# Performance work log

Measured on AMD Instinct MI355X. Metric: run time of the kernel, lower is better.

## Reference

```python
import jax, jax.numpy as jnp
import numpy as np

D_MODEL = 1024
NUM_HEADS = 16
D_K = D_MODEL // NUM_HEADS
LN_EPS = 1e-5
NEG = -1e9


def setup_inputs() -> dict:
    key = jax.random.key(0)
    ks = jax.random.split(key, 12)
    B, S, D = 8, 1024, D_MODEL
    lim = 1.0 / np.sqrt(D)
    def lin(k):
        k1, k2 = jax.random.split(k)
        W = jax.random.uniform(k1, (D, D), jnp.float32, -lim, lim)
        b = jax.random.uniform(k2, (D,), jnp.float32, -lim, lim)
        return W, b
    Wq, bq = lin(ks[0])
    Wk, bk = lin(ks[1])
    Wv, bv = lin(ks[2])
    Wo, bo = lin(ks[3])
    return {
        "history_items": jax.random.normal(ks[4], (B, S, D), jnp.float32),
        "sequence_mask": jax.random.randint(ks[5], (B, S), 0, 2, jnp.int32),
        "Wq": Wq, "bq": bq, "Wk": Wk, "bk": bk,
        "Wv": Wv, "bv": bv, "Wo": Wo, "bo": bo,
        "ln_gamma": jnp.ones((D,), jnp.float32),
        "ln_beta": jnp.zeros((D,), jnp.float32),
    }


def reference(history_items, sequence_mask, Wq, bq, Wk, bk, Wv, bv, Wo, bo, ln_gamma, ln_beta):
    B, S, D = history_items.shape
    H, dk = NUM_HEADS, D_K
    # projections -> [B, H, S, dk]
    def proj(W, b):
        return (history_items @ W.T + b).reshape(B, S, H, dk).transpose(0, 2, 1, 3)
    q = proj(Wq, bq)
    k = proj(Wk, bk)
    v = proj(Wv, bv)
    # combined mask: causal [1,1,S,S] AND key-padding [B,1,1,S]
    causal = jnp.tril(jnp.ones((S, S), bool))[None, None]
    mask = jnp.logical_and(causal, (sequence_mask != 0)[:, None, None, :])
    scores = jnp.einsum('bhqd,bhkd->bhqk', q, k) / np.sqrt(dk).astype(np.float32)
    scores = jnp.where(mask, scores, NEG)
    attn = jax.nn.softmax(scores, axis=-1)
    ctx = jnp.einsum('bhqk,bhkd->bhqd', attn, v)  # [B,H,S,dk]
    concat = ctx.transpose(0, 2, 1, 3).reshape(B, S, D)
    out = concat @ Wo.T + bo
    x = out + history_items
    mu = jnp.mean(x, axis=-1, keepdims=True)
    var = jnp.mean((x - mu) ** 2, axis=-1, keepdims=True)
    return (x - mu) * jax.lax.rsqrt(var + LN_EPS) * ln_gamma + ln_beta
```

## Files before the change

### kernel.cpp

```cpp
#include <hip/hip_runtime.h>
#include <hip/hip_bf16.h>

#define B_ 8
#define S_ 1024
#define D_ 1024
#define H_ 16
#define DK_ 64
#define M_ (B_*S_)

#define QSCALE 0.1803368801111904f

typedef __attribute__((ext_vector_type(4))) float f32x4;
typedef __attribute__((ext_vector_type(8))) short bf16x8;
typedef __attribute__((ext_vector_type(4))) short s16x4;
typedef __hip_bfloat16 bf16;
typedef unsigned long long ull;

#define GLOAD_LDS16(gp, lp) __builtin_amdgcn_global_load_lds( \
    (const __attribute__((address_space(1))) void*)(gp), \
    (__attribute__((address_space(3))) void*)(lp), 16, 0, 0)

#define SBAR()   asm volatile("s_barrier" ::: "memory")
#define VMCNT(n) asm volatile("s_waitcnt vmcnt(" #n ")" ::: "memory")

__device__ __forceinline__ bf16x8 ld8(const bf16* p){ return *(const bf16x8*)p; }

__device__ __forceinline__ short bf16bits(float f){
  bf16 h = __float2bfloat16(f);
  return __builtin_bit_cast(short, h);
}
__device__ __forceinline__ float tof(short b){
  unsigned u = ((unsigned)(unsigned short)b) << 16;
  return __builtin_bit_cast(float, u);
}

__device__ __forceinline__ bf16x8 ld8swz(const bf16* base, int row, int colb){
  int sw = colb ^ ((row & 7) << 4);
  return *(const bf16x8*)((const char*)base + row*128 + sw);
}

template<int CTRL>
__device__ __forceinline__ float dppadd(float x){
  int m = __builtin_amdgcn_update_dpp(0, __builtin_bit_cast(int,x), CTRL, 0xF, 0xF, true);
  return x + __builtin_bit_cast(float,m);
}
__device__ __forceinline__ float red16add(float x){
  x = dppadd<0xB1>(x);
  x = dppadd<0x4E>(x);
  x = dppadd<0x141>(x);
  x = dppadd<0x140>(x);
  return x;
}

__global__ __launch_bounds__(256) void cast_f32_bf16(const float* __restrict__ in,
                                                     bf16* __restrict__ out, int n){
  int i = (blockIdx.x*256 + threadIdx.x)*8;
  if (i >= n) return;
  f32x4 a = *(const f32x4*)(in+i);
  f32x4 b = *(const f32x4*)(in+i+4);
  bf16x8 o;
  #pragma unroll
  for (int c=0;c<4;c++){ o[c] = bf16bits(a[c]); o[c+4] = bf16bits(b[c]); }
  *(bf16x8*)(out+i) = o;
}

__global__ __launch_bounds__(256) void cast_w4(const float* __restrict__ w0, const float* __restrict__ w1,
                                               const float* __restrict__ w2, const float* __restrict__ w3,
                                               bf16* __restrict__ out){
  int sel = blockIdx.x >> 9;
  const float* src = (sel==0)?w0:((sel==1)?w1:((sel==2)?w2:w3));
  int i = (((blockIdx.x & 511)*256) + threadIdx.x)*8;
  f32x4 a = *(const f32x4*)(src+i);
  f32x4 b = *(const f32x4*)(src+i+4);
  bf16x8 o;
  #pragma unroll
  for (int c=0;c<4;c++){ o[c] = bf16bits(a[c]); o[c+4] = bf16bits(b[c]); }
  *(bf16x8*)(out + ((size_t)sel<<20) + i) = o;
}

__global__ __launch_bounds__(256) void vmean_kernel(const bf16* __restrict__ Vt_g,
                                                    float* __restrict__ vmean){
  int r = blockIdx.x*4 + (threadIdx.x>>6);
  int lane = threadIdx.x & 63;
  const bf16* p = Vt_g + (((size_t)r)<<10) + lane*16;
  bf16x8 a = ld8(p), c = ld8(p+8);
  float s = 0.f;
  #pragma unroll
  for (int e=0;e<8;e++) s += tof(a[e]) + tof(c[e]);
  #pragma unroll
  for (int off=1;off<64;off<<=1) s += __shfl_xor(s, off);
  if (lane==0) vmean[r] = s * (1.f/1024.f);
}

template<int MODE>
__global__ __launch_bounds__(256) void gemm128(
    const bf16* __restrict__ A,
    const bf16* __restrict__ W0, const bf16* __restrict__ W1, const bf16* __restrict__ W2,
    const float* __restrict__ b0, const float* __restrict__ b1, const float* __restrict__ b2,
    bf16* __restrict__ o0, bf16* __restrict__ o1, bf16* __restrict__ o2,
    const float* __restrict__ resid, float* __restrict__ xout)
{
  const bf16* Wsel = W0; const float* bsel = b0;
  if (MODE==0){
    int z = blockIdx.z;
    Wsel = (z==0)?W0:((z==1)?W1:W2);
    bsel = (z==0)?b0:((z==1)?b1:b2);
  }
  __shared__ bf16 smem[4*128*64];
  const int tid = threadIdx.x, wid = tid>>6, lane = tid&63;
  const int lr = lane&15, lg = lane>>4;
  const int m0 = blockIdx.x*128, n0 = blockIdx.y*128;
  const int wr = wid>>1, wc = wid&1;
  f32x4 acc[4][4] = {};

  auto STAGE = [&](int k0, int bsel_){
    #pragma unroll
    for (int c=0;c<4;c++){
      int ldsoff = ((c<<2)|wid)<<10;
      int off = ldsoff + (lane<<4);
      int row = off>>7;
      int colb = (off&127) ^ ((row&7)<<4);
      GLOAD_LDS16(A   + (((size_t)(m0+row))<<10) + k0 + (colb>>1), (char*)smem + bsel_*32768 + ldsoff);
      GLOAD_LDS16(Wsel+ (((size_t)(n0+row))<<10) + k0 + (colb>>1), (char*)smem + bsel_*32768 + 16384 + ldsoff);
    }
  };

  STAGE(0, 0);
  int cur = 0;
  for (int kt=0; kt<16; kt++){
    if (kt < 15){ STAGE((kt+1)<<6, cur^1); VMCNT(8); }
    else        { VMCNT(0); }
    SBAR();
    __builtin_amdgcn_sched_barrier(0);
    const bf16* Asb = smem + cur*16384;
    const bf16* Bsb = Asb + 8192;
    bf16x8 af[4][2], bfv[4][2];
    #pragma unroll
    for (int m=0;m<4;m++){
      int row = wr*64 + m*16 + lr;
      af[m][0] = ld8swz(Asb, row, lg*16);
      af[m][1] = ld8swz(Asb, row, lg*16 + 64);
    }
    #pragma unroll
    for (int n=0;n<4;n++){
      int row = wc*64 + n*16 + lr;
      bfv[n][0] = ld8swz(Bsb, row, lg*16);
      bfv[n][1] = ld8swz(Bsb, row, lg*16 + 64);
    }
    #pragma unroll
    for (int m=0;m<4;m++)
      #pragma unroll
      for (int n=0;n<4;n++){
        acc[m][n] = __builtin_amdgcn_mfma_f32_16x16x32_bf16(af[m][0], bfv[n][0], acc[m][n],0,0,0);
        acc[m][n] = __builtin_amdgcn_mfma_f32_16x16x32_bf16(af[m][1], bfv[n][1], acc[m][n],0,0,0);
      }
    __builtin_amdgcn_sched_barrier(0);
    SBAR();
    cur ^= 1;
  }

  if (MODE==0){
    if (blockIdx.z == 2){
      __syncthreads();
      #pragma unroll
      for (int n=0;n<4;n++){
        int c = wc*64 + n*16 + lr;
        float bias = bsel[n0 + c];
        #pragma unroll
        for (int m=0;m<4;m++){
          int r0 = wr*64 + m*16 + lg*4;
          s16x4 pk;
          #pragma unroll
          for (int j=0;j<4;j++) pk[j] = bf16bits(acc[m][n][j] + bias);
          *(s16x4*)((char*)smem + c*256 + ((r0*2) ^ ((c&7)<<4))) = pk;
        }
      }
      __syncthreads();
      #pragma unroll
      for (int q=0;q<8;q++){
        int idx = tid + q*256;
        int c = idx>>4, r8 = idx&15;
        bf16x8 vv = *(const bf16x8*)((char*)smem + c*256 + ((r8*16) ^ ((c&7)<<4)));
        int col = n0 + c;  int h = col>>6, dd = col&63;
        int row0 = m0 + r8*8;  int bb = row0>>10, s0 = row0&1023;
        *(bf16x8*)(o2 + ((((size_t)bb*H_ + h)*DK_ + dd)<<10) + s0) = vv;
      }
    } else {
      bf16* osel = (blockIdx.z==0) ? o0 : o1;
      const float qs = (blockIdx.z==0) ? QSCALE : 1.0f;
      #pragma unroll
      for (int n=0;n<4;n++){
        int col = n0 + wc*64 + n*16 + lr;
        float bias = bsel[col];
        int h = col>>6, dd = col&63;
        #pragma unroll
        for (int m=0;m<4;m++)
          #pragma unroll
          for (int j=0;j<4;j++){
            int row = m0 + wr*64 + m*16 + lg*4 + j;
            int bb = row>>10, s = row&1023;
            osel[((((size_t)bb*H_ + h)<<10) + s)*DK_ + dd] = __float2bfloat16((acc[m][n][j] + bias)*qs);
          }
      }
    }
  } else {
    #pragma unroll
    for (int n=0;n<4;n++){
      int col = n0 + wc*64 + n*16 + lr;
      float bias = bsel[col];
      #pragma unroll
      for (int m=0;m<4;m++)
        #pragma unroll
        for (int j=0;j<4;j++){
          int row = m0 + wr*64 + m*16 + lg*4 + j;
          size_t idx = (((size_t)row)<<10) + col;
          xout[idx] = acc[m][n][j] + bias + resid[idx];
        }
    }
  }
}

__global__ __launch_bounds__(512) void attn_kernel(
    const bf16* __restrict__ Q, const bf16* __restrict__ K, const bf16* __restrict__ Vt_g,
    const int* __restrict__ seqm, const float* __restrict__ vmean, bf16* __restrict__ ctxout)
{
  __shared__ bf16 Ks[2][64*64];
  __shared__ bf16 Vs[2][64*64];
  __shared__ bf16 Ps[8][32*72];
  __shared__ int msk[1024];
  const int tid = threadIdx.x, wid = tid>>6, lane = tid&63;
  const int lr = lane&15, lg = lane>>4;
  const int bh = blockIdx.x, xb = blockIdx.y;
  const int b = bh>>4, h = bh&15;
  const bf16* Qb  = Q    + (size_t)bh * S_ * DK_;
  const bf16* Kb  = K    + (size_t)bh * S_ * DK_;
  const bf16* Vtb = Vt_g + (size_t)bh * DK_ * S_;
  for (int i=tid;i<1024;i+=512) msk[i] = seqm[b*1024+i];

  const int g0 = 8*xb + wid;
  const int rb0 = g0*16;
  const int rb1 = (63 - g0)*16;
  bf16x8 qf[2][2];
  {
    const bf16* p0 = Qb + (size_t)(rb0+lr)*DK_ + lg*8;
    const bf16* p1 = Qb + (size_t)(rb1+lr)*DK_ + lg*8;
    qf[0][0] = ld8(p0); qf[0][1] = ld8(p0+32);
    qf[1][0] = ld8(p1); qf[1][1] = ld8(p1+32);
  }
  f32x4 cacc[2][4] = {};
  float lsum[2][4] = {};

  auto STAGE = [&](int t, int bsel){
    const int j0 = t*64;
    int off = (wid<<10) + (lane<<4);
    int row = off>>7;
    int colb = (off&127) ^ ((row&7)<<4);
    GLOAD_LDS16(Kb  + (size_t)(j0+row)*DK_ + (colb>>1), (char*)&Ks[bsel][0] + (wid<<10));
    GLOAD_LDS16(Vtb + (((size_t)row)<<10) + j0 + (colb>>1), (char*)&Vs[bsel][0] + (wid<<10));
  };

  STAGE(0, 0);
  __syncthreads();

  ull mbits = 0;
  #pragma unroll
  for (int i=0;i<64;i++) mbits |= ((ull)(msk[i*16+lr]!=0)) << i;

  const int bnt = ((1023 - 128*xb) >> 6) + 1;

  int cur = 0;
  for (int t=0; t<bnt; t++){
    if (t+1 < bnt) STAGE(t+1, cur^1);
    const int j0 = t*64;
    if (j0 <= rb1 + 15){
      const bool act0 = (j0 <= rb0 + 15);
      bf16x8 kf[4][2];
      #pragma unroll
      for (int nf=0;nf<4;nf++){
        kf[nf][0] = ld8swz(&Ks[cur][0], nf*16+lr, lg*16);
        kf[nf][1] = ld8swz(&Ks[cur][0], nf*16+lr, lg*16 + 64);
      }
      float madd[4];
      #pragma unroll
      for (int nf=0;nf<4;nf++)
        madd[nf] = ((mbits >> (t*4 + nf)) & 1ull) ? 0.f : -1.0e9f;

      #pragma unroll
      for (int mf=0;mf<2;mf++){
        if (mf==0 && !act0) continue;
        const int rbm = mf ? rb1 : rb0;
        const bool diag = (j0 + 63 > rbm);
        f32x4 sc[4] = {};
        #pragma unroll
        for (int nf=0;nf<4;nf++){
          sc[nf] = __builtin_amdgcn_mfma_f32_16x16x32_bf16(qf[mf][0], kf[nf][0], sc[nf],0,0,0);
          sc[nf] = __builtin_amdgcn_mfma_f32_16x16x32_bf16(qf[mf][1], kf[nf][1], sc[nf],0,0,0);
        }
        #pragma unroll
        for (int j=0;j<4;j++){
          int row = rbm + lg*4 + j;
          float ps = 0.f;
          #pragma unroll
          for (int nf=0;nf<4;nf++){
            float s = sc[nf][j] + madd[nf];
            if (diag){
              int col = j0 + nf*16 + lr;
              s = (col <= row) ? s : -1.0e9f;
            }
            float p = exp2f(s);
            sc[nf][j] = p;
            ps += p;
          }
          lsum[mf][j] += ps;
        }
        #pragma unroll
        for (int nf=0;nf<4;nf++)
          #pragma unroll
          for (int j=0;j<4;j++)
            Ps[wid][(mf*16+lg*4+j)*72 + nf*16+lr] = __float2bfloat16(sc[nf][j]);
      }
      bf16x8 pf[2][2];
      #pragma unroll
      for (int mf=0;mf<2;mf++){
        if (mf==0 && !act0) continue;
        const bf16* p = &Ps[wid][(mf*16+lr)*72 + lg*8];
        pf[mf][0] = *(const bf16x8*)p; pf[mf][1] = *(const bf16x8*)(p+32);
      }
      #pragma unroll
      for (int df=0;df<4;df++){
        #pragma unroll
        for (int kk=0;kk<2;kk++){
          bf16x8 vf = ld8swz(&Vs[cur][0], df*16+lr, lg*16 + kk*64);
          if (act0)
            cacc[0][df] = __builtin_amdgcn_mfma_f32_16x16x32_bf16(pf[0][kk], vf, cacc[0][df],0,0,0);
          cacc[1][df] = __builtin_amdgcn_mfma_f32_16x16x32_bf16(pf[1][kk], vf, cacc[1][df],0,0,0);
        }
      }
    }
    __syncthreads();
    cur ^= 1;
  }

  #pragma unroll
  for (int mf=0;mf<2;mf++){
    const int rbm = mf ? rb1 : rb0;
    float lt[4];
    #pragma unroll
    for (int j=0;j<4;j++) lt[j] = red16add(lsum[mf][j]);
    #pragma unroll
    for (int df=0;df<4;df++)
      #pragma unroll
      for (int j=0;j<4;j++){
        int srow = rbm + lg*4 + j;
        int dd = df*16 + lr;
        float v = cacc[mf][df][j] / lt[j];
        if (lt[j] <= 1.0e-30f) v = vmean[bh*64 + dd];
        ctxout[((size_t)b*S_ + srow)*D_ + h*DK_ + dd] = __float2bfloat16(v);
      }
  }
}

__global__ __launch_bounds__(256) void ln_kernel(const float* __restrict__ X2,
    const float* __restrict__ gamma, const float* __restrict__ beta, float* __restrict__ out)
{
  const int row = blockIdx.x, tid = threadIdx.x;
  const int lane = tid&63, wid = tid>>6;
  const f32x4* xr = (const f32x4*)(X2 + (((size_t)row)<<10));
  f32x4 v = xr[tid];
  float s  = v[0]+v[1]+v[2]+v[3];
  float s2 = v[0]*v[0]+v[1]*v[1]+v[2]*v[2]+v[3]*v[3];
  #pragma unroll
  for (int off=1;off<64;off<<=1){ s += __shfl_xor(s,off); s2 += __shfl_xor(s2,off); }
  __shared__ float red[8];
  if (lane==0){ red[wid]=s; red[wid+4]=s2; }
  __syncthreads();
  s  = red[0]+red[1]+red[2]+red[3];
  s2 = red[4]+red[5]+red[6]+red[7];
  float mu  = s*(1.f/1024.f);
  float var = s2*(1.f/1024.f) - mu*mu;
  float inv = rsqrtf(var + 1e-5f);
  f32x4 gv = ((const f32x4*)gamma)[tid], bv = ((const f32x4*)beta)[tid];
  f32x4 o;
  #pragma unroll
  for (int c=0;c<4;c++) o[c] = (v[c]-mu)*inv*gv[c] + bv[c];
  ((f32x4*)(out + (((size_t)row)<<10)))[tid] = o;
}

extern "C" void kernel_launch(void* const* d_in, const int* in_sizes, int n_in,
                              void* d_out, int out_size, void* d_ws, size_t ws_size,
                              hipStream_t stream) {
  const float* X   = (const float*)d_in[0];
  const int*   sm  = (const int*)d_in[1];
  const float* Wq  = (const float*)d_in[2];  const float* bq = (const float*)d_in[3];
  const float* Wk  = (const float*)d_in[4];  const float* bk = (const float*)d_in[5];
  const float* Wv  = (const float*)d_in[6];  const float* bv = (const float*)d_in[7];
  const float* Wo  = (const float*)d_in[8];  const float* bo = (const float*)d_in[9];
  const float* ga  = (const float*)d_in[10]; const float* be = (const float*)d_in[11];
  float* out = (float*)d_out;
  char* ws = (char*)d_ws;

  bf16* Xbf = (bf16*)(ws);
  bf16* Wqb = (bf16*)(ws + (16u<<20));
  bf16* Wkb = (bf16*)(ws + (18u<<20));
  bf16* Wvb = (bf16*)(ws + (20u<<20));
  bf16* Wob = (bf16*)(ws + (22u<<20));
  bf16* Qh  = (bf16*)(ws + (24u<<20));
  bf16* Kh  = (bf16*)(ws + (40u<<20));
  bf16* Vth = (bf16*)(ws + (56u<<20));
  bf16* Ctx = (bf16*)(ws + (72u<<20));
  float* X2 = (float*)(ws + (24u<<20));
  float* vmean = (float*)(ws + (16u<<20));

  cast_f32_bf16<<<4096,256,0,stream>>>(X,  Xbf, M_*D_);
  cast_w4<<<2048,256,0,stream>>>(Wq, Wk, Wv, Wo, Wqb);

  dim3 g1(M_/128, D_/128, 3);
  gemm128<0><<<g1,256,0,stream>>>(Xbf, Wqb,Wkb,Wvb, bq,bk,bv, Qh,Kh,Vth, nullptr, nullptr);

  vmean_kernel<<<B_*H_*DK_/4,256,0,stream>>>(Vth, vmean);

  dim3 g2(B_*H_, 4);
  attn_kernel<<<g2,512,0,stream>>>(Qh, Kh, Vth, sm, vmean, Ctx);

  dim3 g3(M_/128, D_/128, 1);
  gemm128<1><<<g3,256,0,stream>>>(Ctx, Wob,nullptr,nullptr, bo,nullptr,nullptr,
                                  nullptr,nullptr,nullptr, X, X2);

  ln_kernel<<<M_,256,0,stream>>>(X2, ga, be, out);
}
```

Measured before the change: 182.1 us.

## Load K/V fragments directly from global memory per wave, dropping LDS staging

The attention kernel no longer stages K and V tiles into double-buffered shared memory with block-wide barriers. Each wave now reads its K and V^T MFMA fragments straight from global memory (through L2/L1) and runs only as many tiles as its own causal range needs, so per-tile __syncthreads disappears and waves proceed independently. It also raises wave priority around the PV MFMAs. The cost is redundant global/L2 traffic, since eight waves each load the same K/V tiles, and no explicit prefetch to hide load latency.

```diff
diff --git a/kernel.cpp b/kernel.cpp
--- a/kernel.cpp
+++ b/kernel.cpp
@@ -224,8 +224,6 @@
     const bf16* __restrict__ Q, const bf16* __restrict__ K, const bf16* __restrict__ Vt_g,
     const int* __restrict__ seqm, const float* __restrict__ vmean, bf16* __restrict__ ctxout)
 {
-  __shared__ bf16 Ks[2][64*64];
-  __shared__ bf16 Vs[2][64*64];
   __shared__ bf16 Ps[8][32*72];
   __shared__ int msk[1024];
   const int tid = threadIdx.x, wid = tid>>6, lane = tid&63;
@@ -250,95 +248,93 @@
   f32x4 cacc[2][4] = {};
   float lsum[2][4] = {};
 
-  auto STAGE = [&](int t, int bsel){
+  __syncthreads();
+
+  ull mbits = 0;
+  #pragma unroll
+  for (int i=0;i<64;i++) mbits |= ((ull)(msk[i*16+lr]!=0)) << i;
+
+  const int ntw = ((rb1 + 15) >> 6) + 1;
+
+  for (int t=0; t<ntw; t++){
     const int j0 = t*64;
-    int off = (wid<<10) + (lane<<4);
-    int row = off>>7;
-    int colb = (off&127) ^ ((row&7)<<4);
-    GLOAD_LDS16(Kb  + (size_t)(j0+row)*DK_ + (colb>>1), (char*)&Ks[bsel][0] + (wid<<10));
-    GLOAD_LDS16(Vtb + (((size_t)row)<<10) + j0 + (colb>>1), (char*)&Vs[bsel][0] + (wid<<10));
-  };
-
-  STAGE(0, 0);
-  __syncthreads();
-
-  ull mbits = 0;
-  #pragma unroll
-  for (int i=0;i<64;i++) mbits |= ((ull)(msk[i*16+lr]!=0)) << i;
-
-  const int bnt = ((1023 - 128*xb) >> 6) + 1;
-
-  int cur = 0;
-  for (int t=0; t<bnt; t++){
-    if (t+1 < bnt) STAGE(t+1, cur^1);
-    const int j0 = t*64;
-    if (j0 <= rb1 + 15){
-      const bool act0 = (j0 <= rb0 + 15);
-      bf16x8 kf[4][2];
+    const bool act0 = (j0 <= rb0 + 15);
+
+    bf16x8 kf[4][2];
+    #pragma unroll
+    for (int nf=0;nf<4;nf++){
+      const bf16* kp = Kb + (size_t)(j0 + nf*16 + lr)*DK_ + lg*8;
+      kf[nf][0] = ld8(kp); kf[nf][1] = ld8(kp+32);
+    }
+
+    float madd[4];
+    #pragma unroll
+    for (int nf=0;nf<4;nf++)
+      madd[nf] = ((mbits >> (t*4 + nf)) & 1ull) ? 0.f : -1.0e9f;
+
+    #pragma unroll
+    for (int mf=0;mf<2;mf++){
+      if (mf==0 && !act0) continue;
+      const int rbm = mf ? rb1 : rb0;
+      const bool diag = (j0 + 63 > rbm);
+      f32x4 sc[4] = {};
       #pragma unroll
       for (int nf=0;nf<4;nf++){
-        kf[nf][0] = ld8swz(&Ks[cur][0], nf*16+lr, lg*16);
-        kf[nf][1] = ld8swz(&Ks[cur][0], nf*16+lr, lg*16 + 64);
-      }
-      float madd[4];
+        sc[nf] = __builtin_amdgcn_mfma_f32_16x16x32_bf16(qf[mf][0], kf[nf][0], sc[nf],0,0,0);
+        sc[nf] = __builtin_amdgcn_mfma_f32_16x16x32_bf16(qf[mf][1], kf[nf][1], sc[nf],0,0,0);
+      }
+      #pragma unroll
+      for (int j=0;j<4;j++){
+        int row = rbm + lg*4 + j;
+        float ps = 0.f;
+        #pragma unroll
+        for (int nf=0;nf<4;nf++){
+          float s = sc[nf][j] + madd[nf];
+          if (diag){
+            int col = j0 + nf*16 + lr;
+            s = (col <= row) ? s : -1.0e9f;
+          }
+          float p = exp2f(s);
+          sc[nf][j] = p;
+          ps += p;
+        }
+        lsum[mf][j] += ps;
+      }
       #pragma unroll
       for (int nf=0;nf<4;nf++)
-        madd[nf] = ((mbits >> (t*4 + nf)) & 1ull) ? 0.f : -1.0e9f;
-
-      #pragma unroll
-      for (int mf=0;mf<2;mf++){
-        if (mf==0 && !act0) continue;
-        const int rbm = mf ? rb1 : rb0;
-        const bool diag = (j0 + 63 > rbm);
-        f32x4 sc[4] = {};
-        #pragma unroll
-        for (int nf=0;nf<4;nf++){
-          sc[nf] = __builtin_amdgcn_mfma_f32_16x16x32_bf16(qf[mf][0], kf[nf][0], sc[nf],0,0,0);
-          sc[nf] = __builtin_amdgcn_mfma_f32_16x16x32_bf16(qf[mf][1], kf[nf][1], sc[nf],0,0,0);
+        #pragma unroll
+        for (int j=0;j<4;j++)
+          Ps[wid][(mf*16+lg*4+j)*72 + nf*16+lr] = __float2bfloat16(sc[nf][j]);
+    }
+
+    bf16x8 pf[2][2];
+    #pragma unroll
+    for (int mf=0;mf<2;mf++){
+      if (mf==0 && !act0) continue;
+      const bf16* p = &Ps[wid][(mf*16+lr)*72 + lg*8];
+      pf[mf][0] = *(const bf16x8*)p; pf[mf][1] = *(const bf16x8*)(p+32);
+    }
+
+    #pragma unroll
+    for (int half=0;half<2;half++){
+      bf16x8 vf[2][2];
+      #pragma unroll
+      for (int df=0;df<2;df++){
+        const bf16* vp = Vtb + (size_t)((half*2+df)*16+lr)*S_ + j0 + lg*8;
+        vf[df][0] = ld8(vp); vf[df][1] = ld8(vp+32);
+      }
+      __builtin_amdgcn_s_setprio(1);
+      #pragma unroll
+      for (int df=0;df<2;df++){
+        #pragma unroll
+        for (int kk=0;kk<2;kk++){
+          if (act0)
+            cacc[0][half*2+df] = __builtin_amdgcn_mfma_f32_16x16x32_bf16(pf[0][kk], vf[df][kk], cacc[0][half*2+df],0,0,0);
+          cacc[1][half*2+df] = __builtin_amdgcn_mfma_f32_16x16x32_bf16(pf[1][kk], vf[df][kk], cacc[1][half*2+df],0,0,0);
         }
-        #pragma unroll
-        for (int j=0;j<4;j++){
-          int row = rbm + lg*4 + j;
-          float ps = 0.f;
-          #pragma unroll
-          for (int nf=0;nf<4;nf++){
-            float s = sc[nf][j] + madd[nf];
-            if (diag){
-              int col = j0 + nf*16 + lr;
-              s = (col <= row) ? s : -1.0e9f;
-            }
-            float p = exp2f(s);
-            sc[nf][j] = p;
-            ps += p;
-          }
-          lsum[mf][j] += ps;
-        }
-        #pragma unroll
-        for (int nf=0;nf<4;nf++)
-          #pragma unroll
-          for (int j=0;j<4;j++)
-            Ps[wid][(mf*16+lg*4+j)*72 + nf*16+lr] = __float2bfloat16(sc[nf][j]);
-      }
-      bf16x8 pf[2][2];
-      #pragma unroll
-      for (int mf=0;mf<2;mf++){
-        if (mf==0 && !act0) continue;
-        const bf16* p = &Ps[wid][(mf*16+lr)*72 + lg*8];
-        pf[mf][0] = *(const bf16x8*)p; pf[mf][1] = *(const bf16x8*)(p+32);
-      }
-      #pragma unroll
-      for (int df=0;df<4;df++){
-        #pragma unroll
-        for (int kk=0;kk<2;kk++){
-          bf16x8 vf = ld8swz(&Vs[cur][0], df*16+lr, lg*16 + kk*64);
-          if (act0)
-            cacc[0][df] = __builtin_amdgcn_mfma_f32_16x16x32_bf16(pf[0][kk], vf, cacc[0][df],0,0,0);
-          cacc[1][df] = __builtin_amdgcn_mfma_f32_16x16x32_bf16(pf[1][kk], vf, cacc[1][df],0,0,0);
-        }
-      }
-    }
-    __syncthreads();
-    cur ^= 1;
+      }
+      __builtin_amdgcn_s_setprio(0);
+    }
   }
 
   #pragma unroll
```

Result: slower. 218.2 us (+19.9%).

## Split attention into one query tile per warp with register-staged K/V

Applied to the files above, without the earlier changes.

The attention kernel no longer pairs a front and back query tile per warp for causal load balancing. It now launches 8 blocks per batch-head, each warp handling a single 16-row tile and each block iterating only over the key tiles it needs. K/V staging moves from async global-to-LDS double buffering to a single LDS buffer fed by register prefetch. The P buffer and mask use less LDS, and launch bounds request 3 blocks per CU to raise occupancy. In exchange, causal work is unbalanced across blocks and each tile iteration now needs an extra barrier.

```diff
diff --git a/kernel.cpp b/kernel.cpp
--- a/kernel.cpp
+++ b/kernel.cpp
@@ -220,144 +220,135 @@
   }
 }
 
-__global__ __launch_bounds__(512) void attn_kernel(
+__global__ __launch_bounds__(512, 3) void attn_kernel(
     const bf16* __restrict__ Q, const bf16* __restrict__ K, const bf16* __restrict__ Vt_g,
     const int* __restrict__ seqm, const float* __restrict__ vmean, bf16* __restrict__ ctxout)
 {
-  __shared__ bf16 Ks[2][64*64];
-  __shared__ bf16 Vs[2][64*64];
-  __shared__ bf16 Ps[8][32*72];
-  __shared__ int msk[1024];
+  __shared__ bf16 Ks[64*64];
+  __shared__ bf16 Vs[64*64];
+  __shared__ bf16 Ps[8][16*64];
+  __shared__ unsigned char mskb[1024];
   const int tid = threadIdx.x, wid = tid>>6, lane = tid&63;
   const int lr = lane&15, lg = lane>>4;
-  const int bh = blockIdx.x, xb = blockIdx.y;
+  const int xb = blockIdx.x, bh = blockIdx.y;
   const int b = bh>>4, h = bh&15;
   const bf16* Qb  = Q    + (size_t)bh * S_ * DK_;
   const bf16* Kb  = K    + (size_t)bh * S_ * DK_;
   const bf16* Vtb = Vt_g + (size_t)bh * DK_ * S_;
-  for (int i=tid;i<1024;i+=512) msk[i] = seqm[b*1024+i];
+  for (int i=tid;i<1024;i+=512) mskb[i] = (unsigned char)(seqm[b*1024+i]!=0);
 
   const int g0 = 8*xb + wid;
-  const int rb0 = g0*16;
-  const int rb1 = (63 - g0)*16;
-  bf16x8 qf[2][2];
+  const int rb = g0*16;
+  bf16x8 qf[2];
   {
-    const bf16* p0 = Qb + (size_t)(rb0+lr)*DK_ + lg*8;
-    const bf16* p1 = Qb + (size_t)(rb1+lr)*DK_ + lg*8;
-    qf[0][0] = ld8(p0); qf[0][1] = ld8(p0+32);
-    qf[1][0] = ld8(p1); qf[1][1] = ld8(p1+32);
+    const bf16* p0 = Qb + (size_t)(rb+lr)*DK_ + lg*8;
+    qf[0] = ld8(p0); qf[1] = ld8(p0+32);
   }
-  f32x4 cacc[2][4] = {};
-  float lsum[2][4] = {};
-
-  auto STAGE = [&](int t, int bsel){
+  f32x4 cacc[4] = {};
+  float lsum[4] = {};
+
+  const int srow = tid>>3;
+  const int scolb = (tid&7)*16;
+  const int ssw = scolb ^ ((srow&7)<<4);
+  bf16x8 kr, vr;
+  auto STAGE_LOAD = [&](int t){
     const int j0 = t*64;
-    int off = (wid<<10) + (lane<<4);
-    int row = off>>7;
-    int colb = (off&127) ^ ((row&7)<<4);
-    GLOAD_LDS16(Kb  + (size_t)(j0+row)*DK_ + (colb>>1), (char*)&Ks[bsel][0] + (wid<<10));
-    GLOAD_LDS16(Vtb + (((size_t)row)<<10) + j0 + (colb>>1), (char*)&Vs[bsel][0] + (wid<<10));
+    kr = ld8(Kb  + (size_t)(j0+srow)*DK_ + (scolb>>1));
+    vr = ld8(Vtb + (((size_t)srow)<<10) + j0 + (scolb>>1));
   };
-
-  STAGE(0, 0);
+  auto STAGE_WRITE = [&](){
+    *(bf16x8*)((char*)Ks + srow*128 + ssw) = kr;
+    *(bf16x8*)((char*)Vs + srow*128 + ssw) = vr;
+  };
+
+  const int bnt = 2*xb + 2;
+
+  STAGE_LOAD(0);
+  STAGE_WRITE();
+  if (bnt > 1) STAGE_LOAD(1);
   __syncthreads();
 
   ull mbits = 0;
   #pragma unroll
-  for (int i=0;i<64;i++) mbits |= ((ull)(msk[i*16+lr]!=0)) << i;
-
-  const int bnt = ((1023 - 128*xb) >> 6) + 1;
-
-  int cur = 0;
+  for (int i=0;i<64;i++) mbits |= ((ull)mskb[i*16+lr]) << i;
+
   for (int t=0; t<bnt; t++){
-    if (t+1 < bnt) STAGE(t+1, cur^1);
     const int j0 = t*64;
-    if (j0 <= rb1 + 15){
-      const bool act0 = (j0 <= rb0 + 15);
+    if (j0 <= rb + 15){
       bf16x8 kf[4][2];
       #pragma unroll
       for (int nf=0;nf<4;nf++){
-        kf[nf][0] = ld8swz(&Ks[cur][0], nf*16+lr, lg*16);
-        kf[nf][1] = ld8swz(&Ks[cur][0], nf*16+lr, lg*16 + 64);
+        kf[nf][0] = ld8swz(Ks, nf*16+lr, lg*16);
+        kf[nf][1] = ld8swz(Ks, nf*16+lr, lg*16 + 64);
       }
       float madd[4];
       #pragma unroll
       for (int nf=0;nf<4;nf++)
         madd[nf] = ((mbits >> (t*4 + nf)) & 1ull) ? 0.f : -1.0e9f;
 
-      #pragma unroll
-      for (int mf=0;mf<2;mf++){
-        if (mf==0 && !act0) continue;
-        const int rbm = mf ? rb1 : rb0;
-        const bool diag = (j0 + 63 > rbm);
-        f32x4 sc[4] = {};
+      const bool diag = (j0 + 63 > rb);
+      f32x4 sc[4] = {};
+      #pragma unroll
+      for (int nf=0;nf<4;nf++){
+        sc[nf] = __builtin_amdgcn_mfma_f32_16x16x32_bf16(qf[0], kf[nf][0], sc[nf],0,0,0);
+        sc[nf] = __builtin_amdgcn_mfma_f32_16x16x32_bf16(qf[1], kf[nf][1], sc[nf],0,0,0);
+      }
+      #pragma unroll
+      for (int j=0;j<4;j++){
+        int row = rb + lg*4 + j;
+        float ps = 0.f;
         #pragma unroll
         for (int nf=0;nf<4;nf++){
-          sc[nf] = __builtin_amdgcn_mfma_f32_16x16x32_bf16(qf[mf][0], kf[nf][0], sc[nf],0,0,0);
-          sc[nf] = __builtin_amdgcn_mfma_f32_16x16x32_bf16(qf[mf][1], kf[nf][1], sc[nf],0,0,0);
+          float s = sc[nf][j] + madd[nf];
+          if (diag){
+            int col = j0 + nf*16 + lr;
+            s = (col <= row) ? s : -1.0e9f;
+          }
+          float p = exp2f(s);
+          sc[nf][j] = p;
+          ps += p;
         }
+        lsum[j] += ps;
+      }
+      char* pbase = (char*)&Ps[wid][0];
+      #pragma unroll
+      for (int nf=0;nf<4;nf++)
         #pragma unroll
         for (int j=0;j<4;j++){
-          int row = rbm + lg*4 + j;
-          float ps = 0.f;
-          #pragma unroll
-          for (int nf=0;nf<4;nf++){
-            float s = sc[nf][j] + madd[nf];
-            if (diag){
-              int col = j0 + nf*16 + lr;
-              s = (col <= row) ? s : -1.0e9f;
-            }
-            float p = exp2f(s);
-            sc[nf][j] = p;
-            ps += p;
-          }
-          lsum[mf][j] += ps;
+          int prow = lg*4 + j;
+          *(short*)(pbase + prow*128 + (((nf*16+lr)*2) ^ ((prow&7)<<4))) = bf16bits(sc[nf][j]);
         }
-        #pragma unroll
-        for (int nf=0;nf<4;nf++)
-          #pragma unroll
-          for (int j=0;j<4;j++)
-            Ps[wid][(mf*16+lg*4+j)*72 + nf*16+lr] = __float2bfloat16(sc[nf][j]);
-      }
-      bf16x8 pf[2][2];
-      #pragma unroll
-      for (int mf=0;mf<2;mf++){
-        if (mf==0 && !act0) continue;
-        const bf16* p = &Ps[wid][(mf*16+lr)*72 + lg*8];
-        pf[mf][0] = *(const bf16x8*)p; pf[mf][1] = *(const bf16x8*)(p+32);
-      }
+      bf16x8 pf0 = ld8swz(&Ps[wid][0], lr, lg*16);
+      bf16x8 pf1 = ld8swz(&Ps[wid][0], lr, lg*16 + 64);
       #pragma unroll
       for (int df=0;df<4;df++){
-        #pragma unroll
-        for (int kk=0;kk<2;kk++){
-          bf16x8 vf = ld8swz(&Vs[cur][0], df*16+lr, lg*16 + kk*64);
-          if (act0)
-            cacc[0][df] = __builtin_amdgcn_mfma_f32_16x16x32_bf16(pf[0][kk], vf, cacc[0][df],0,0,0);
-          cacc[1][df] = __builtin_amdgcn_mfma_f32_16x16x32_bf16(pf[1][kk], vf, cacc[1][df],0,0,0);
-        }
+        bf16x8 vf0 = ld8swz(Vs, df*16+lr, lg*16);
+        bf16x8 vf1 = ld8swz(Vs, df*16+lr, lg*16 + 64);
+        cacc[df] = __builtin_amdgcn_mfma_f32_16x16x32_bf16(pf0, vf0, cacc[df],0,0,0);
+        cacc[df] = __builtin_amdgcn_mfma_f32_16x16x32_bf16(pf1, vf1, cacc[df],0,0,0);
       }
     }
     __syncthreads();
-    cur ^= 1;
+    if (t+1 < bnt){
+      STAGE_WRITE();
+      if (t+2 < bnt) STAGE_LOAD(t+2);
+      __syncthreads();
+    }
   }
 
-  #pragma unroll
-  for (int mf=0;mf<2;mf++){
-    const int rbm = mf ? rb1 : rb0;
-    float lt[4];
-    #pragma unroll
-    for (int j=0;j<4;j++) lt[j] = red16add(lsum[mf][j]);
-    #pragma unroll
-    for (int df=0;df<4;df++)
-      #pragma unroll
-      for (int j=0;j<4;j++){
-        int srow = rbm + lg*4 + j;
-        int dd = df*16 + lr;
-        float v = cacc[mf][df][j] / lt[j];
-        if (lt[j] <= 1.0e-30f) v = vmean[bh*64 + dd];
-        ctxout[((size_t)b*S_ + srow)*D_ + h*DK_ + dd] = __float2bfloat16(v);
-      }
-  }
+  float lt[4];
+  #pragma unroll
+  for (int j=0;j<4;j++) lt[j] = red16add(lsum[j]);
+  #pragma unroll
+  for (int df=0;df<4;df++)
+    #pragma unroll
+    for (int j=0;j<4;j++){
+      int srow2 = rb + lg*4 + j;
+      int dd = df*16 + lr;
+      float v = cacc[df][j] / lt[j];
+      if (lt[j] <= 1.0e-30f) v = vmean[bh*64 + dd];
+      ctxout[((size_t)b*S_ + srow2)*D_ + h*DK_ + dd] = __float2bfloat16(v);
+    }
 }
 
 __global__ __launch_bounds__(256) void ln_kernel(const float* __restrict__ X2,
@@ -419,7 +410,7 @@
 
   vmean_kernel<<<B_*H_*DK_/4,256,0,stream>>>(Vth, vmean);
 
-  dim3 g2(B_*H_, 4);
+  dim3 g2(8, B_*H_);
   attn_kernel<<<g2,512,0,stream>>>(Qh, Kh, Vth, sm, vmean, Ctx);
 
   dim3 g3(M_/128, D_/128, 1);
```

Result: slower. 198.3 us (+8.9%).
